# Optimization experiments

Hardware: AMD Instinct MI355X
Metric: run time of the kernel (lower is better)

Reference implementation:

```python
import jax, jax.numpy as jnp
import numpy as np

N_NODES = 50000
N_EDGES = 1600000
D_FEAT = 64
N_SCALARS = 4
N_GRAPHS = 64
HIDDEN = 128
OUT = 128


def setup_inputs() -> dict:
    key = jax.random.key(0)
    ks = jax.random.split(key, 8)
    x = jax.random.normal(ks[0], (N_NODES, D_FEAT), dtype=jnp.float32)
    scalars = jax.random.normal(ks[1], (N_GRAPHS, N_SCALARS), dtype=jnp.float32)
    batch = jnp.sort(jax.random.randint(ks[2], (N_NODES,), 0, N_GRAPHS))
    edge_index = jax.random.randint(ks[3], (2, N_EDGES), 0, N_NODES)
    d_in = 2 * (D_FEAT + N_SCALARS)  # 136: EdgeConv-style cat([x_i, x_j - x_i])
    W1 = jax.random.normal(ks[4], (d_in, HIDDEN), dtype=jnp.float32) * (1.0 / np.sqrt(d_in))
    b1 = jnp.zeros((HIDDEN,), dtype=jnp.float32)
    W2 = jax.random.normal(ks[5], (HIDDEN, OUT), dtype=jnp.float32) * (1.0 / np.sqrt(HIDDEN))
    b2 = jnp.zeros((OUT,), dtype=jnp.float32)
    return {"x": x, "scalars": scalars, "batch": batch, "edge_index": edge_index,
            "W1": W1, "b1": b1, "W2": W2, "b2": b2}


def reference(x, scalars, batch, edge_index, W1, b1, W2, b2):
    # _reshape_scalars: gather per-graph scalars to nodes via batch index
    s = scalars[batch]                       # [N, n_scalars]
    h = jnp.concatenate([x, s], axis=-1)     # [N, d_feat + n_scalars]
    src, dst = edge_index[0], edge_index[1]  # edge j -> i (PyG convention)
    h_i = h[dst]                             # target node features [E, F]
    h_j = h[src]                             # source node features [E, F]
    m_in = jnp.concatenate([h_i, h_j - h_i], axis=-1)  # [E, 2F]
    m = jax.nn.relu(m_in @ W1 + b1) @ W2 + b2          # edge MLP [E, OUT]
    out = jax.ops.segment_sum(m, dst, num_segments=x.shape[0])  # add-aggregation
    return out
```

## Files before the change

### kernel.cpp

```cpp
#include <hip/hip_runtime.h>

#define N_NODES   50000
#define N_EDGES   1600000
#define D_FEAT    64
#define N_SCALARS 4
#define HIDDEN    128
#define OUT_DIM   128
#define UV_DIM    256

#define SLICE_SH  6
#define SLICE_N   (1 << SLICE_SH)
#define NSLICE    ((N_NODES + SLICE_N - 1) >> SLICE_SH)
#define CAP       2560
#define CHUNK     4096

#define N_WAVES   (N_NODES / 16)
#define G1_BLOCKS ((N_WAVES + 3) / 4)
#define BIN_BLOCKS ((N_EDGES + CHUNK - 1) / CHUNK)

typedef __attribute__((ext_vector_type(8))) _Float16 half8;
typedef __attribute__((ext_vector_type(2))) _Float16 half2v;
typedef __attribute__((ext_vector_type(4))) float    f32x4;

__device__ __forceinline__ float wf_elem(const float* W1, int k, int j) {
    float wb = W1[(k + 68) * HIDDEN + (j & 127)];
    return (j < HIDDEN) ? (W1[k * HIDDEN + j] - wb) : wb;
}

__global__ __launch_bounds__(256) void prep_kernel(
    const float* __restrict__ W1, const float* __restrict__ b1,
    const float* __restrict__ W2, const float* __restrict__ scalars,
    _Float16* __restrict__ WfT, _Float16* __restrict__ W2T,
    float* __restrict__ SG, int* __restrict__ tails)
{
    const int idx = blockIdx.x * 256 + threadIdx.x;
    {   int j = idx >> 6, k = idx & 63;
        WfT[idx] = (_Float16)wf_elem(W1, k, j); }
    {   int j = idx >> 7, k = idx & 127;
        W2T[idx] = (_Float16)W2[k * OUT_DIM + j]; }
    {   int g = idx >> 8, j = idx & 255;
        float s = (j < HIDDEN) ? b1[j] : 0.f;
        #pragma unroll
        for (int t = 0; t < N_SCALARS; ++t)
            s = fmaf(scalars[g * N_SCALARS + t], wf_elem(W1, D_FEAT + t, j), s);
        SG[idx] = s; }
    if (idx < NSLICE) tails[idx] = 0;
}

__global__ __launch_bounds__(256) void gemm1_bin(
    const float* __restrict__ x, const int* __restrict__ batch,
    const _Float16* __restrict__ WfT, const float* __restrict__ SG,
    _Float16* __restrict__ Uh, _Float16* __restrict__ Vh,
    const int* __restrict__ ei, int* __restrict__ tails,
    unsigned* __restrict__ glist)
{
    __shared__ unsigned buf[CHUNK];
    __shared__ int hist[NSLICE];
    __shared__ int binStart[NSLICE];
    __shared__ int cursor[NSLICE];
    __shared__ int gbase[NSLICE];
    __shared__ int scanTmp[256];

    const int tid = threadIdx.x;

    if (blockIdx.x < G1_BLOCKS) {
        const int wid = (blockIdx.x * 256 + tid) >> 6;
        if (wid >= N_WAVES) return;
        const int lane = tid & 63;
        const int quad = lane >> 4;
        const int l15  = lane & 15;
        const int row0 = wid * 16;

        f32x4 acc[16];
        #pragma unroll
        for (int c = 0; c < 16; ++c) { f32x4 z = {0.f,0.f,0.f,0.f}; acc[c] = z; }

        const float* xrow = x + (row0 + l15) * D_FEAT;
        #pragma unroll
        for (int t = 0; t < 2; ++t) {
            const int k0 = 32 * t + quad * 8;
            float4 a0 = *(const float4*)(xrow + k0);
            float4 a1 = *(const float4*)(xrow + k0 + 4);
            half8 af;
            af[0] = (_Float16)a0.x; af[1] = (_Float16)a0.y;
            af[2] = (_Float16)a0.z; af[3] = (_Float16)a0.w;
            af[4] = (_Float16)a1.x; af[5] = (_Float16)a1.y;
            af[6] = (_Float16)a1.z; af[7] = (_Float16)a1.w;
            #pragma unroll
            for (int c = 0; c < 16; ++c) {
                half8 bf = *(const half8*)(WfT + (c * 16 + l15) * 64 + k0);
                acc[c] = __builtin_amdgcn_mfma_f32_16x16x32_f16(af, bf, acc[c], 0, 0, 0);
            }
        }

        int bg[4];
        #pragma unroll
        for (int j = 0; j < 4; ++j) bg[j] = batch[row0 + quad * 4 + j];

        #pragma unroll
        for (int c = 0; c < 16; ++c) {
            const int col = c * 16 + l15;
            #pragma unroll
            for (int j = 0; j < 4; ++j) {
                const int n = row0 + quad * 4 + j;
                float v = acc[c][j] + SG[bg[j] * UV_DIM + col];
                if (col < HIDDEN) Uh[(n << 7) + col] = (_Float16)v;
                else              Vh[(n << 7) + col - HIDDEN] = (_Float16)v;
            }
        }
        return;
    }

    const int e0  = (blockIdx.x - G1_BLOCKS) * CHUNK;
    const int nE  = min(CHUNK, N_EDGES - e0);

    for (int i = tid; i < NSLICE; i += 256) hist[i] = 0;
    __syncthreads();

    unsigned ent[CHUNK / 256];
    #pragma unroll
    for (int j = 0; j < CHUNK / 256; ++j) {
        int e = e0 + tid + j * 256;
        if (e < N_EDGES) {
            unsigned s = (unsigned)ei[e];
            unsigned d = (unsigned)ei[N_EDGES + e];
            ent[j] = (d << 16) | s;
            atomicAdd(&hist[d >> SLICE_SH], 1);
        } else {
            ent[j] = 0xFFFFFFFFu;
        }
    }
    __syncthreads();

    const int base4 = tid * 4;
    int loc[4];
    int sum = 0;
    #pragma unroll
    for (int k = 0; k < 4; ++k) {
        int b = base4 + k;
        loc[k] = (b < NSLICE) ? hist[b] : 0;
        sum += loc[k];
    }
    scanTmp[tid] = sum;
    __syncthreads();
    for (int d = 1; d < 256; d <<= 1) {
        int v = (tid >= d) ? scanTmp[tid - d] : 0;
        __syncthreads();
        scanTmp[tid] += v;
        __syncthreads();
    }
    int run = (tid == 0) ? 0 : scanTmp[tid - 1];
    #pragma unroll
    for (int k = 0; k < 4; ++k) {
        int b = base4 + k;
        if (b < NSLICE) { binStart[b] = run; cursor[b] = run; run += loc[k]; }
    }
    __syncthreads();

    #pragma unroll
    for (int j = 0; j < CHUNK / 256; ++j) {
        if (ent[j] != 0xFFFFFFFFu) {
            int sl = (int)(ent[j] >> (16 + SLICE_SH));
            int pos = atomicAdd(&cursor[sl], 1);
            buf[pos] = ent[j];
        }
    }
    __syncthreads();

    for (int s = tid; s < NSLICE; s += 256) {
        int c = hist[s];
        if (c > 0) gbase[s] = atomicAdd(&tails[s], c);
    }
    __syncthreads();

    for (int i = tid; i < nE; i += 256) {
        unsigned e = buf[i];
        int sl = (int)(e >> (16 + SLICE_SH));
        int di = gbase[sl] + (i - binStart[sl]);
        if (di < CAP) glist[(size_t)sl * CAP + di] = e;
    }
}

__global__ __launch_bounds__(256) void aggregate_slice(
    const unsigned* __restrict__ glist, const int* __restrict__ tails,
    const _Float16* __restrict__ Uh, const _Float16* __restrict__ Vh,
    _Float16* __restrict__ aggh, int* __restrict__ deg)
{
    __shared__ int h64[64];
    __shared__ int start64[64];
    __shared__ int cur64[64];
    __shared__ int scanB[64];
    __shared__ unsigned sbuf[CAP];

    const int slice = blockIdx.x;
    const int node0 = slice << SLICE_SH;
    const int tid   = threadIdx.x;
    const unsigned* lst = glist + (size_t)slice * CAP;
    const int cnt = min(tails[slice], CAP);

    if (tid < 64) h64[tid] = 0;
    __syncthreads();
    for (int i = tid; i < cnt; i += 256)
        atomicAdd(&h64[(lst[i] >> 16) & 63], 1);
    __syncthreads();
    if (tid < 64) scanB[tid] = h64[tid];
    __syncthreads();
    for (int d = 1; d < 64; d <<= 1) {
        int v = 0;
        if (tid < 64 && tid >= d) v = scanB[tid - d];
        __syncthreads();
        if (tid < 64) scanB[tid] += v;
        __syncthreads();
    }
    if (tid < 64) {
        start64[tid] = scanB[tid] - h64[tid];
        cur64[tid]   = scanB[tid] - h64[tid];
    }
    __syncthreads();
    for (int i = tid; i < cnt; i += 256) {
        unsigned e = lst[i];
        int dl = (e >> 16) & 63;
        int p = atomicAdd(&cur64[dl], 1);
        sbuf[p] = e & 0xFFFFu;
    }
    __syncthreads();

    const int wave = tid >> 6;
    const int lane = tid & 63;
    const int c2   = lane * 2;
    const half2v zero = {(_Float16)0, (_Float16)0};

    for (int dl = wave + 4 * blockIdx.y; dl < 64; dl += 8) {
        int n = node0 + dl;
        if (n >= N_NODES) continue;
        const int gb = start64[dl];
        const int gc = h64[dl];
        const half2v u2 = *(const half2v*)(Uh + (n << 7) + c2);
        half2v acc2 = zero;

        int p = gb, pe = gb + gc;
        for (; p + 8 <= pe; p += 8) {
            int s0 = sbuf[p + 0], s1 = sbuf[p + 1];
            int s2 = sbuf[p + 2], s3 = sbuf[p + 3];
            int s4 = sbuf[p + 4], s5 = sbuf[p + 5];
            int s6 = sbuf[p + 6], s7 = sbuf[p + 7];
            half2v v0 = *(const half2v*)(Vh + (s0 << 7) + c2);
            half2v v1 = *(const half2v*)(Vh + (s1 << 7) + c2);
            half2v v2 = *(const half2v*)(Vh + (s2 << 7) + c2);
            half2v v3 = *(const half2v*)(Vh + (s3 << 7) + c2);
            half2v v4 = *(const half2v*)(Vh + (s4 << 7) + c2);
            half2v v5 = *(const half2v*)(Vh + (s5 << 7) + c2);
            half2v v6 = *(const half2v*)(Vh + (s6 << 7) + c2);
            half2v v7 = *(const half2v*)(Vh + (s7 << 7) + c2);
            half2v m0 = __builtin_elementwise_max(u2 + v0, zero);
            half2v m1 = __builtin_elementwise_max(u2 + v1, zero);
            half2v m2 = __builtin_elementwise_max(u2 + v2, zero);
            half2v m3 = __builtin_elementwise_max(u2 + v3, zero);
            half2v m4 = __builtin_elementwise_max(u2 + v4, zero);
            half2v m5 = __builtin_elementwise_max(u2 + v5, zero);
            half2v m6 = __builtin_elementwise_max(u2 + v6, zero);
            half2v m7 = __builtin_elementwise_max(u2 + v7, zero);
            acc2 += ((m0 + m1) + (m2 + m3)) + ((m4 + m5) + (m6 + m7));
        }
        for (; p < pe; ++p) {
            int s0 = sbuf[p];
            half2v v0 = *(const half2v*)(Vh + (s0 << 7) + c2);
            acc2 += __builtin_elementwise_max(u2 + v0, zero);
        }
        *(half2v*)(aggh + (n << 7) + c2) = acc2;
        if (lane == 0) deg[n] = gc;
    }
}

__global__ __launch_bounds__(256) void gemm2_mfma(
    const _Float16* __restrict__ aggh, const int* __restrict__ deg,
    const _Float16* __restrict__ W2T, const float* __restrict__ b2,
    float* __restrict__ out)
{
    const int wid = (blockIdx.x * 256 + threadIdx.x) >> 6;
    if (wid >= N_WAVES) return;
    const int lane = threadIdx.x & 63;
    const int quad = lane >> 4;
    const int l15  = lane & 15;
    const int row0 = wid * 16;

    f32x4 acc[8];
    #pragma unroll
    for (int c = 0; c < 8; ++c) { f32x4 z = {0.f,0.f,0.f,0.f}; acc[c] = z; }

    const _Float16* arow = aggh + ((row0 + l15) << 7);
    #pragma unroll
    for (int t = 0; t < 4; ++t) {
        const int k0 = 32 * t + quad * 8;
        half8 af = *(const half8*)(arow + k0);
        #pragma unroll
        for (int c = 0; c < 8; ++c) {
            half8 bf = *(const half8*)(W2T + ((c * 16 + l15) << 7) + k0);
            acc[c] = __builtin_amdgcn_mfma_f32_16x16x32_f16(af, bf, acc[c], 0, 0, 0);
        }
    }

    int dg[4];
    #pragma unroll
    for (int j = 0; j < 4; ++j) dg[j] = deg[row0 + quad * 4 + j];

    #pragma unroll
    for (int c = 0; c < 8; ++c) {
        const int col = c * 16 + l15;
        const float bb = b2[col];
        #pragma unroll
        for (int j = 0; j < 4; ++j) {
            const int n = row0 + quad * 4 + j;
            out[(size_t)n * OUT_DIM + col] = acc[c][j] + bb * (float)dg[j];
        }
    }
}

extern "C" void kernel_launch(void* const* d_in, const int* in_sizes, int n_in,
                              void* d_out, int out_size, void* d_ws, size_t ws_size,
                              hipStream_t stream)
{
    const float* x       = (const float*)d_in[0];
    const float* scalars = (const float*)d_in[1];
    const int*   batch   = (const int*)d_in[2];
    const int*   ei      = (const int*)d_in[3];
    const float* W1      = (const float*)d_in[4];
    const float* b1      = (const float*)d_in[5];
    const float* W2      = (const float*)d_in[6];
    const float* b2      = (const float*)d_in[7];
    float*       out     = (float*)d_out;

    _Float16* Uh    = (_Float16*)d_ws;
    _Float16* Vh    = Uh + (size_t)N_NODES * HIDDEN;
    _Float16* aggh  = Vh + (size_t)N_NODES * HIDDEN;
    unsigned* glist = (unsigned*)(aggh + (size_t)N_NODES * HIDDEN);
    _Float16* WfT   = (_Float16*)(glist + (size_t)NSLICE * CAP);
    _Float16* W2T   = WfT + 256 * 64;
    float*    SG    = (float*)(W2T + 128 * 128);
    int*      deg   = (int*)(SG + 64 * UV_DIM);
    int*      tails = deg + N_NODES;

    prep_kernel<<<64, 256, 0, stream>>>(W1, b1, W2, scalars, WfT, W2T, SG, tails);

    gemm1_bin<<<G1_BLOCKS + BIN_BLOCKS, 256, 0, stream>>>(
        x, batch, WfT, SG, Uh, Vh, ei, tails, glist);

    aggregate_slice<<<dim3(NSLICE, 2), 256, 0, stream>>>(
        glist, tails, Uh, Vh, aggh, deg);

    gemm2_mfma<<<(N_WAVES * 64 + 255) / 256, 256, 0, stream>>>(
        aggh, deg, W2T, b2, out);
}
```

Baseline: 207.3 us.

## Fuse slice aggregation with second GEMM through shared-memory tile

Merges the aggregation and the W2 MFMA GEMM into one kernel. Each block now handles 16 nodes of a 64-node slice and keeps the aggregated fp16 rows in LDS, so the aggh and deg buffers are never written to or read back from global memory and one launch is dropped. The per-node edge lists are padded to 4-entry alignment so source indices can be read from LDS with vector loads. In exchange, each of the four blocks per slice rescans the whole slice edge list, each block performs only a small 16-row GEMM, and per-quarter lists longer than 1024 edges are truncated.

```diff
diff --git a/kernel.cpp b/kernel.cpp
--- a/kernel.cpp
+++ b/kernel.cpp
@@ -12,6 +12,7 @@
 #define SLICE_N   (1 << SLICE_SH)
 #define NSLICE    ((N_NODES + SLICE_N - 1) >> SLICE_SH)
 #define CAP       2560
+#define CAPQ      1024
 #define CHUNK     4096
 
 #define N_WAVES   (N_NODES / 16)
@@ -181,77 +182,81 @@
     }
 }
 
-__global__ __launch_bounds__(256) void aggregate_slice(
+__global__ __launch_bounds__(256) void agg_gemm2(
     const unsigned* __restrict__ glist, const int* __restrict__ tails,
     const _Float16* __restrict__ Uh, const _Float16* __restrict__ Vh,
-    _Float16* __restrict__ aggh, int* __restrict__ deg)
+    const _Float16* __restrict__ W2T, const float* __restrict__ b2,
+    float* __restrict__ out)
 {
-    __shared__ int h64[64];
-    __shared__ int start64[64];
-    __shared__ int cur64[64];
-    __shared__ int scanB[64];
-    __shared__ unsigned sbuf[CAP];
+    __shared__ int h16[16];
+    __shared__ int start16[16];
+    __shared__ int cur16[16];
+    __shared__ unsigned sbuf[CAPQ];
+    __shared__ _Float16 aggA[16][136];
 
     const int slice = blockIdx.x;
-    const int node0 = slice << SLICE_SH;
+    const int yq    = blockIdx.y;
+    const int node0 = (slice << SLICE_SH) + yq * 16;
     const int tid   = threadIdx.x;
     const unsigned* lst = glist + (size_t)slice * CAP;
     const int cnt = min(tails[slice], CAP);
 
-    if (tid < 64) h64[tid] = 0;
-    __syncthreads();
-    for (int i = tid; i < cnt; i += 256)
-        atomicAdd(&h64[(lst[i] >> 16) & 63], 1);
-    __syncthreads();
-    if (tid < 64) scanB[tid] = h64[tid];
-    __syncthreads();
-    for (int d = 1; d < 64; d <<= 1) {
-        int v = 0;
-        if (tid < 64 && tid >= d) v = scanB[tid - d];
-        __syncthreads();
-        if (tid < 64) scanB[tid] += v;
-        __syncthreads();
-    }
-    if (tid < 64) {
-        start64[tid] = scanB[tid] - h64[tid];
-        cur64[tid]   = scanB[tid] - h64[tid];
-    }
+    if (tid < 16) h16[tid] = 0;
     __syncthreads();
     for (int i = tid; i < cnt; i += 256) {
         unsigned e = lst[i];
         int dl = (e >> 16) & 63;
-        int p = atomicAdd(&cur64[dl], 1);
-        sbuf[p] = e & 0xFFFFu;
+        if ((dl >> 4) == yq) atomicAdd(&h16[dl & 15], 1);
+    }
+    __syncthreads();
+    if (tid == 0) {
+        int run = 0;
+        #pragma unroll
+        for (int b = 0; b < 16; ++b) {
+            run = (run + 3) & ~3;
+            start16[b] = run; cur16[b] = run;
+            run += h16[b];
+        }
+    }
+    __syncthreads();
+    for (int i = tid; i < cnt; i += 256) {
+        unsigned e = lst[i];
+        int dl = (e >> 16) & 63;
+        if ((dl >> 4) == yq) {
+            int pos = atomicAdd(&cur16[dl & 15], 1);
+            if (pos < CAPQ) sbuf[pos] = e & 0xFFFFu;
+        }
     }
     __syncthreads();
 
     const int wave = tid >> 6;
     const int lane = tid & 63;
+    const int quad = lane >> 4;
+    const int l15  = lane & 15;
     const int c2   = lane * 2;
     const half2v zero = {(_Float16)0, (_Float16)0};
 
-    for (int dl = wave + 4 * blockIdx.y; dl < 64; dl += 8) {
-        int n = node0 + dl;
-        if (n >= N_NODES) continue;
-        const int gb = start64[dl];
-        const int gc = h64[dl];
-        const half2v u2 = *(const half2v*)(Uh + (n << 7) + c2);
-        half2v acc2 = zero;
-
-        int p = gb, pe = gb + gc;
+    #pragma unroll
+    for (int i = 0; i < 4; ++i) {
+        const int b = wave * 4 + i;
+        const int n = node0 + b;
+        half2v u2 = zero, acc2 = zero;
+        int gb = start16[b];
+        int gc = h16[b];
+        if (n < N_NODES) u2 = *(const half2v*)(Uh + (n << 7) + c2);
+        else gc = 0;
+        int p = gb, pe = min(gb + gc, CAPQ);
         for (; p + 8 <= pe; p += 8) {
-            int s0 = sbuf[p + 0], s1 = sbuf[p + 1];
-            int s2 = sbuf[p + 2], s3 = sbuf[p + 3];
-            int s4 = sbuf[p + 4], s5 = sbuf[p + 5];
-            int s6 = sbuf[p + 6], s7 = sbuf[p + 7];
-            half2v v0 = *(const half2v*)(Vh + (s0 << 7) + c2);
-            half2v v1 = *(const half2v*)(Vh + (s1 << 7) + c2);
-            half2v v2 = *(const half2v*)(Vh + (s2 << 7) + c2);
-            half2v v3 = *(const half2v*)(Vh + (s3 << 7) + c2);
-            half2v v4 = *(const half2v*)(Vh + (s4 << 7) + c2);
-            half2v v5 = *(const half2v*)(Vh + (s5 << 7) + c2);
-            half2v v6 = *(const half2v*)(Vh + (s6 << 7) + c2);
-            half2v v7 = *(const half2v*)(Vh + (s7 << 7) + c2);
+            uint4 q0 = *(const uint4*)&sbuf[p];
+            uint4 q1 = *(const uint4*)&sbuf[p + 4];
+            half2v v0 = *(const half2v*)(Vh + (q0.x << 7) + c2);
+            half2v v1 = *(const half2v*)(Vh + (q0.y << 7) + c2);
+            half2v v2 = *(const half2v*)(Vh + (q0.z << 7) + c2);
+            half2v v3 = *(const half2v*)(Vh + (q0.w << 7) + c2);
+            half2v v4 = *(const half2v*)(Vh + (q1.x << 7) + c2);
+            half2v v5 = *(const half2v*)(Vh + (q1.y << 7) + c2);
+            half2v v6 = *(const half2v*)(Vh + (q1.z << 7) + c2);
+            half2v v7 = *(const half2v*)(Vh + (q1.w << 7) + c2);
             half2v m0 = __builtin_elementwise_max(u2 + v0, zero);
             half2v m1 = __builtin_elementwise_max(u2 + v1, zero);
             half2v m2 = __builtin_elementwise_max(u2 + v2, zero);
@@ -262,56 +267,52 @@
             half2v m7 = __builtin_elementwise_max(u2 + v7, zero);
             acc2 += ((m0 + m1) + (m2 + m3)) + ((m4 + m5) + (m6 + m7));
         }
+        for (; p + 4 <= pe; p += 4) {
+            uint4 q0 = *(const uint4*)&sbuf[p];
+            half2v v0 = *(const half2v*)(Vh + (q0.x << 7) + c2);
+            half2v v1 = *(const half2v*)(Vh + (q0.y << 7) + c2);
+            half2v v2 = *(const half2v*)(Vh + (q0.z << 7) + c2);
+            half2v v3 = *(const half2v*)(Vh + (q0.w << 7) + c2);
+            acc2 += (__builtin_elementwise_max(u2 + v0, zero)
+                   + __builtin_elementwise_max(u2 + v1, zero))
+                  + (__builtin_elementwise_max(u2 + v2, zero)
+                   + __builtin_elementwise_max(u2 + v3, zero));
+        }
         for (; p < pe; ++p) {
-            int s0 = sbuf[p];
+            int s0 = (int)sbuf[p];
             half2v v0 = *(const half2v*)(Vh + (s0 << 7) + c2);
             acc2 += __builtin_elementwise_max(u2 + v0, zero);
         }
-        *(half2v*)(aggh + (n << 7) + c2) = acc2;
-        if (lane == 0) deg[n] = gc;
-    }
-}
-
-__global__ __launch_bounds__(256) void gemm2_mfma(
-    const _Float16* __restrict__ aggh, const int* __restrict__ deg,
-    const _Float16* __restrict__ W2T, const float* __restrict__ b2,
-    float* __restrict__ out)
-{
-    const int wid = (blockIdx.x * 256 + threadIdx.x) >> 6;
-    if (wid >= N_WAVES) return;
-    const int lane = threadIdx.x & 63;
-    const int quad = lane >> 4;
-    const int l15  = lane & 15;
-    const int row0 = wid * 16;
-
-    f32x4 acc[8];
-    #pragma unroll
-    for (int c = 0; c < 8; ++c) { f32x4 z = {0.f,0.f,0.f,0.f}; acc[c] = z; }
-
-    const _Float16* arow = aggh + ((row0 + l15) << 7);
+        *(half2v*)&aggA[b][c2] = acc2;
+    }
+    __syncthreads();
+
+    f32x4 accm[2];
+    {   f32x4 z = {0.f,0.f,0.f,0.f}; accm[0] = z; accm[1] = z; }
     #pragma unroll
     for (int t = 0; t < 4; ++t) {
         const int k0 = 32 * t + quad * 8;
-        half8 af = *(const half8*)(arow + k0);
-        #pragma unroll
-        for (int c = 0; c < 8; ++c) {
-            half8 bf = *(const half8*)(W2T + ((c * 16 + l15) << 7) + k0);
-            acc[c] = __builtin_amdgcn_mfma_f32_16x16x32_f16(af, bf, acc[c], 0, 0, 0);
-        }
-    }
-
-    int dg[4];
-    #pragma unroll
-    for (int j = 0; j < 4; ++j) dg[j] = deg[row0 + quad * 4 + j];
-
-    #pragma unroll
-    for (int c = 0; c < 8; ++c) {
-        const int col = c * 16 + l15;
+        half8 af = *(const half8*)&aggA[l15][k0];
+        #pragma unroll
+        for (int c = 0; c < 2; ++c) {
+            const int ct = wave * 2 + c;
+            half8 bf = *(const half8*)(W2T + ((ct * 16 + l15) << 7) + k0);
+            accm[c] = __builtin_amdgcn_mfma_f32_16x16x32_f16(af, bf, accm[c], 0, 0, 0);
+        }
+    }
+    int dgj[4];
+    #pragma unroll
+    for (int j = 0; j < 4; ++j) dgj[j] = h16[quad * 4 + j];
+
+    #pragma unroll
+    for (int c = 0; c < 2; ++c) {
+        const int col = (wave * 2 + c) * 16 + l15;
         const float bb = b2[col];
         #pragma unroll
         for (int j = 0; j < 4; ++j) {
-            const int n = row0 + quad * 4 + j;
-            out[(size_t)n * OUT_DIM + col] = acc[c][j] + bb * (float)dg[j];
+            const int n = node0 + quad * 4 + j;
+            if (n < N_NODES)
+                out[(size_t)n * OUT_DIM + col] = accm[c][j] + bb * (float)dgj[j];
         }
     }
 }
@@ -332,22 +333,17 @@
 
     _Float16* Uh    = (_Float16*)d_ws;
     _Float16* Vh    = Uh + (size_t)N_NODES * HIDDEN;
-    _Float16* aggh  = Vh + (size_t)N_NODES * HIDDEN;
-    unsigned* glist = (unsigned*)(aggh + (size_t)N_NODES * HIDDEN);
+    unsigned* glist = (unsigned*)(Vh + (size_t)N_NODES * HIDDEN);
     _Float16* WfT   = (_Float16*)(glist + (size_t)NSLICE * CAP);
     _Float16* W2T   = WfT + 256 * 64;
     float*    SG    = (float*)(W2T + 128 * 128);
-    int*      deg   = (int*)(SG + 64 * UV_DIM);
-    int*      tails = deg + N_NODES;
+    int*      tails = (int*)(SG + 64 * UV_DIM);
 
     prep_kernel<<<64, 256, 0, stream>>>(W1, b1, W2, scalars, WfT, W2T, SG, tails);
 
     gemm1_bin<<<G1_BLOCKS + BIN_BLOCKS, 256, 0, stream>>>(
         x, batch, WfT, SG, Uh, Vh, ei, tails, glist);
 
-    aggregate_slice<<<dim3(NSLICE, 2), 256, 0, stream>>>(
-        glist, tails, Uh, Vh, aggh, deg);
-
-    gemm2_mfma<<<(N_WAVES * 64 + 255) / 256, 256, 0, stream>>>(
-        aggh, deg, W2T, b2, out);
-}
+    agg_gemm2<<<dim3(NSLICE, 4), 256, 0, stream>>>(
+        glist, tails, Uh, Vh, W2T, b2, out);
+}
```

Result: faster. 196.9 us (-5.0%).
